# Optimization experiments

Hardware: AMD Instinct MI355X
Metric: run time of the kernel (lower is better)

Reference implementation:

```python
import jax, jax.numpy as jnp
import numpy as np

L, B, H, NI, V = 256, 32, 1024, 1024, 10000


def setup_inputs() -> dict:
    key = jax.random.key(0)
    ks = jax.random.split(key, 8)
    return {
        "input_ids": jax.random.randint(ks[0], (L, B), 0, V),
        "h0": jnp.zeros((B, H), jnp.float32),
        "c0": jnp.zeros((B, H), jnp.float32),
        "emb_w": jax.random.uniform(ks[1], (V, NI), jnp.float32, -0.1, 0.1),
        "w_ih": jax.random.normal(ks[2], (4 * H, NI), jnp.float32) * 0.02,
        "w_hh": jax.random.normal(ks[3], (4 * H, H), jnp.float32) * 0.02,
        "dec_w": jax.random.uniform(ks[4], (V, H), jnp.float32, -0.1, 0.1),
        "dec_b": jnp.zeros((V,), jnp.float32),
        "W": jax.random.normal(ks[5], (H, 1), jnp.float32) * 0.1,
        "U": jax.random.normal(ks[6], (H, 1), jnp.float32) * 0.1,
    }


def reference(input_ids, h0, c0, emb_w, w_ih, w_hh, dec_w, dec_b, W, U):
    seq_len, bsz = input_ids.shape
    nhid = h0.shape[1]
    emb = emb_w[input_ids]  # [L, B, NI]

    def lstm_cell(x, h, c):
        # torch LSTMCell (bias=False), gate order i, f, g, o
        gates = x @ w_ih.T + h @ w_hh.T  # [B, 4H]
        i, f, g, o = jnp.split(gates, 4, axis=-1)
        c_new = jax.nn.sigmoid(f) * c + jax.nn.sigmoid(i) * jnp.tanh(g)
        h_new = jax.nn.sigmoid(o) * jnp.tanh(c_new)
        return h_new, c_new

    time_idx = jnp.arange(seq_len)

    def step(carry, xs):
        h, c, hist = carry  # hist: [L, B, H] padded history of hiddens
        x, i = xs
        h, c = lstm_cell(x, h, c)
        hist = hist.at[i].set(h)
        # additive attention over all hiddens so far
        b = (hist.reshape(-1, nhid) @ U).reshape(seq_len, bsz)  # [L, B]
        a = (h @ W).reshape(1, bsz)  # [1, B]
        scores = jnp.tanh(a + b)
        scores = jnp.where((time_idx <= i)[:, None], scores, -jnp.inf)
        att = jax.nn.softmax(scores, axis=0)  # softmax over time
        ctx = jnp.sum(att[:, :, None] * hist, axis=0)  # [B, H]
        return (h, c, hist), ctx

    hist0 = jnp.zeros((seq_len, bsz, nhid), dtype=h0.dtype)
    (h, c, _), ctx = jax.lax.scan(step, (h0, c0, hist0), (emb, time_idx))
    # ctx: [L, B, H]
    logits = ctx @ dec_w.T + dec_b  # [L, B, V]
    out = jax.nn.log_softmax(logits, axis=-1)
    return out, (h, c)
```

## Files before the change

kernel.cpp:

```cpp
#include <hip/hip_runtime.h>
#include <math.h>

typedef unsigned short u16;
typedef unsigned u32;
typedef float f32x4 __attribute__((ext_vector_type(4)));
typedef float f32x2 __attribute__((ext_vector_type(2)));
typedef __bf16 bf16x8 __attribute__((ext_vector_type(8)));
typedef u16 u16x8 __attribute__((ext_vector_type(8)));
typedef u16 u16x4 __attribute__((ext_vector_type(4)));
typedef u32 u32x4 __attribute__((ext_vector_type(4)));

#define L_SEQ 256
#define BSZ 32
#define HID 1024
#define NIN 1024
#define VOC 10000
#define G4 4096
#define MROWS 8192
#define NB 64
#define DPB 16
#define SENT 0xFFFFFFFFu

__device__ __forceinline__ u16 f2bf(float f) {
    unsigned u = __float_as_uint(f);
    unsigned r = u + 0x7FFFu + ((u >> 16) & 1u);
    return (u16)(r >> 16);
}

__device__ __forceinline__ float fast_sigm(float x) {
    x = fminf(fmaxf(x, -15.f), 15.f);
    return __builtin_amdgcn_rcpf(1.f + __expf(-x));
}
__device__ __forceinline__ float fast_tanh(float x) {
    x = fminf(fmaxf(x, -15.f), 15.f);
    float t = __expf(2.f * x);
    return (t - 1.f) * __builtin_amdgcn_rcpf(t + 1.f);
}

__device__ __forceinline__ unsigned umax4(u16x8 v) {
    u32x4 c = __builtin_bit_cast(u32x4, v);
    unsigned a = c.x > c.y ? c.x : c.y;
    unsigned b = c.z > c.w ? c.z : c.w;
    return a > b ? a : b;
}

__global__ __launch_bounds__(256) void cvt_bf16_kernel(const float* __restrict__ in,
                                                       u16* __restrict__ out, int n4) {
    int idx = blockIdx.x * 256 + threadIdx.x;
    if (idx < n4) {
        f32x4 v = *(const f32x4*)(in + (size_t)idx * 4);
        u16x4 o = {f2bf(v.x), f2bf(v.y), f2bf(v.z), f2bf(v.w)};
        *(u16x4*)(out + (size_t)idx * 4) = o;
    }
}

__global__ __launch_bounds__(256) void gather_emb_kernel(const int* __restrict__ ids,
                                                         const float* __restrict__ emb_w,
                                                         u16* __restrict__ out) {
    int m = blockIdx.x;
    int id = ids[m];
    const float* src = emb_w + (size_t)id * NIN;
    u16* dst = out + (size_t)m * NIN;
    int t = threadIdx.x;
    f32x4 v = *(const f32x4*)(src + t * 4);
    u16x4 o = {f2bf(v.x), f2bf(v.y), f2bf(v.z), f2bf(v.w)};
    *(u16x4*)(dst + t * 4) = o;
}

__global__ __launch_bounds__(256) void gemm_bt_kernel(const u16* __restrict__ A,
                                                      const u16* __restrict__ B,
                                                      float* __restrict__ C,
                                                      const float* __restrict__ bias,
                                                      int M, int N, int K) {
    int m0 = blockIdx.x * 128;
    int n0 = blockIdx.y * 128;
    __shared__ alignas(16) u16 As[128][40];
    __shared__ alignas(16) u16 Bs[128][40];
    int t = threadIdx.x;
    int lane = t & 63, wave = t >> 6;
    int wr = wave >> 1, wc = wave & 1;
    int l15 = lane & 15, l4 = lane >> 4;

    f32x4 acc[4][4];
    f32x4 zv = {0.f, 0.f, 0.f, 0.f};
    for (int mi = 0; mi < 4; ++mi)
        for (int ni = 0; ni < 4; ++ni) acc[mi][ni] = zv;

    for (int k0 = 0; k0 < K; k0 += 32) {
        for (int s = 0; s < 2; ++s) {
            int task = t + s * 256;
            int row = task >> 2, kof = (task & 3) * 8;
            u16x8 av = *(const u16x8*)(A + (size_t)(m0 + row) * K + k0 + kof);
            *(u16x8*)(&As[row][kof]) = av;
            int brow = n0 + row;
            u16x8 bv = {0, 0, 0, 0, 0, 0, 0, 0};
            if (brow < N) bv = *(const u16x8*)(B + (size_t)brow * K + k0 + kof);
            *(u16x8*)(&Bs[row][kof]) = bv;
        }
        __syncthreads();
        bf16x8 af[4], bfr[4];
        for (int mi = 0; mi < 4; ++mi)
            af[mi] = __builtin_bit_cast(bf16x8, *(const u16x8*)(&As[wr * 64 + mi * 16 + l15][l4 * 8]));
        for (int ni = 0; ni < 4; ++ni)
            bfr[ni] = __builtin_bit_cast(bf16x8, *(const u16x8*)(&Bs[wc * 64 + ni * 16 + l15][l4 * 8]));
        for (int mi = 0; mi < 4; ++mi)
            for (int ni = 0; ni < 4; ++ni)
                acc[mi][ni] = __builtin_amdgcn_mfma_f32_16x16x32_bf16(af[mi], bfr[ni], acc[mi][ni], 0, 0, 0);
        __syncthreads();
    }

    for (int mi = 0; mi < 4; ++mi)
        for (int ni = 0; ni < 4; ++ni) {
            int col = n0 + wc * 64 + ni * 16 + l15;
            if (col < N) {
                float bb = bias ? bias[col] : 0.f;
                int rbase = m0 + wr * 64 + mi * 16 + l4 * 4;
                for (int r = 0; r < 4; ++r)
                    C[(size_t)(rbase + r) * N + col] = acc[mi][ni][r] + bb;
            }
        }
}


__global__ __launch_bounds__(256, 1) void lstm_seq_kernel(
    const float* __restrict__ c0, const u16* __restrict__ w_hh_bf,
    const float* __restrict__ gx, const float* __restrict__ Wv, const float* __restrict__ Uv,
    float* __restrict__ hist, u16* __restrict__ hb_hist, float* __restrict__ c_out,
    float* __restrict__ part_ab) {
    __shared__ alignas(16) u16 Bs[64][1024];
    __shared__ float gsm[4][32][16];
    __shared__ float c_sl[32][16];

    int blk = blockIdx.x;
    int d0 = blk * DPB;
    int t = threadIdx.x;
    int lane = t & 63, wave = t >> 6;
    int wm = wave & 1, wn = wave >> 1;
    int l15 = lane & 15, l4 = lane >> 4;

    for (int s = 0; s < 32; ++s) {
        int cid = t + s * 256;
        int c = cid >> 7;
        int ch = cid & 127;
        int g = c >> 4, dl = c & 15;
        u16x8 v = *(const u16x8*)(w_hh_bf + (size_t)(g * HID + d0 + dl) * HID + ch * 8);
        int chs = ch ^ (c & 7);
        *(u16x8*)(&Bs[c][chs * 8]) = v;
    }
    for (int s = t; s < 512; s += 256) {
        int b = s >> 4, dl = s & 15;
        c_sl[b][dl] = c0[b * HID + d0 + dl];
    }
    __syncthreads();

    int cA = wn * 32 + l15;
    int cB = cA + 16;
    int sw = cA & 7;
    int gA = cA >> 4, dA = cA & 15;
    int gB = cB >> 4, dB = cB & 15;

    int bb = t >> 3;
    int pr = t & 7;
    int dl0 = pr * 2;

    for (int i = 0; i < L_SEQ; ++i) {
        const u16* hb = hb_hist + (size_t)i * (BSZ * HID);
        const u16* aptr = hb + (size_t)(wm * 16 + l15) * HID + l4 * 8;

        float gxa[2][4];
#pragma unroll
        for (int r = 0; r < 4; ++r) {
            int m = wm * 16 + l4 * 4 + r;
            size_t rowb = (size_t)(i * BSZ + m) * G4;
            gxa[0][r] = gx[rowb + gA * HID + d0 + dA];
            gxa[1][r] = gx[rowb + gB * HID + d0 + dB];
        }

        u16x8 afr[32];
        unsigned needmask = 0xFFFFFFFFu;
        do {
#pragma unroll
            for (int kk = 0; kk < 32; ++kk)
                if (needmask & (1u << kk))
                    asm volatile("global_load_dwordx4 %0, %1, off offset:%c2 sc0 sc1"
                                 : "=v"(afr[kk])
                                 : "v"(aptr), "n"(kk * 64));
            asm volatile("s_waitcnt vmcnt(0)" ::: "memory");
            __builtin_amdgcn_sched_barrier(0);
            unsigned nm = 0;
#pragma unroll
            for (int kk = 0; kk < 32; ++kk)
                if (needmask & (1u << kk)) {
                    if (__ballot(umax4(afr[kk]) == SENT)) nm |= (1u << kk);
                }
            needmask = nm;
            if (needmask) __builtin_amdgcn_s_sleep(1);
        } while (needmask);
        __builtin_amdgcn_sched_barrier(0);

        f32x4 acc0 = {0.f, 0.f, 0.f, 0.f}, acc1 = {0.f, 0.f, 0.f, 0.f};
#pragma unroll
        for (int kk = 0; kk < 32; ++kk) {
            bf16x8 af = __builtin_bit_cast(bf16x8, afr[kk]);
            int ch = kk * 4 + l4;
            bf16x8 b0 = __builtin_bit_cast(bf16x8, *(const u16x8*)(&Bs[cA][(ch ^ sw) * 8]));
            bf16x8 b1 = __builtin_bit_cast(bf16x8, *(const u16x8*)(&Bs[cB][(ch ^ sw) * 8]));
            acc0 = __builtin_amdgcn_mfma_f32_16x16x32_bf16(af, b0, acc0, 0, 0, 0);
            acc1 = __builtin_amdgcn_mfma_f32_16x16x32_bf16(af, b1, acc1, 0, 0, 0);
        }

#pragma unroll
        for (int r = 0; r < 4; ++r) {
            int m = wm * 16 + l4 * 4 + r;
            gsm[gA][m][dA] = acc0[r] + gxa[0][r];
            gsm[gB][m][dB] = acc1[r] + gxa[1][r];
        }
        __syncthreads();

        u16* hb_next = hb_hist + (size_t)(i + 1) * (BSZ * HID);
        float hn01[2];
#pragma unroll
        for (int q = 0; q < 2; ++q) {
            int dl = dl0 + q;
            float ig = gsm[0][bb][dl], fg = gsm[1][bb][dl];
            float gg = gsm[2][bb][dl], og = gsm[3][bb][dl];
            float cn = fast_sigm(fg) * c_sl[bb][dl] + fast_sigm(ig) * fast_tanh(gg);
            float hn = fast_sigm(og) * fast_tanh(cn);
            c_sl[bb][dl] = cn;
            hn01[q] = hn;
        }
        unsigned pk = (unsigned)f2bf(hn01[0]) | ((unsigned)f2bf(hn01[1]) << 16);
        __hip_atomic_store((unsigned*)(hb_next + bb * HID + d0 + dl0), pk,
                           __ATOMIC_RELAXED, __HIP_MEMORY_SCOPE_AGENT);
        f32x2 hv = {hn01[0], hn01[1]};
        *(f32x2*)(hist + ((size_t)i * BSZ + bb) * HID + d0 + dl0) = hv;
        float pa = hn01[0] * Wv[d0 + dl0] + hn01[1] * Wv[d0 + dl0 + 1];
        float pb = hn01[0] * Uv[d0 + dl0] + hn01[1] * Uv[d0 + dl0 + 1];
        pa += __shfl_xor(pa, 1); pb += __shfl_xor(pb, 1);
        pa += __shfl_xor(pa, 2); pb += __shfl_xor(pb, 2);
        pa += __shfl_xor(pa, 4); pb += __shfl_xor(pb, 4);
        if (pr == 0) {
            f32x2 pv = {pa, pb};
            *(f32x2*)(part_ab + (((size_t)i * NB + blk) * BSZ + bb) * 2) = pv;
        }
    }

    for (int s = t; s < 512; s += 256) {
        int b2 = s >> 4, dl = s & 15;
        c_out[b2 * HID + d0 + dl] = c_sl[b2][dl];
    }
}

__global__ __launch_bounds__(256) void reduce_ab_kernel(const float* __restrict__ part_ab,
                                                        float* __restrict__ a_arr,
                                                        float* __restrict__ b_arr) {
    int i = blockIdx.x;
    int t = threadIdx.x;
    int b = t & 31, q = t >> 5;
    float sa = 0.f, sb = 0.f;
    for (int j = 0; j < 8; ++j) {
        int blk = q * 8 + j;
        f32x2 v = *(const f32x2*)(part_ab + (((size_t)i * NB + blk) * BSZ + b) * 2);
        sa += v.x;
        sb += v.y;
    }
    __shared__ float ra[8][32], rb[8][32];
    ra[q][b] = sa;
    rb[q][b] = sb;
    __syncthreads();
    if (q == 0) {
        for (int j = 1; j < 8; ++j) { sa += ra[j][b]; sb += rb[j][b]; }
        a_arr[i * BSZ + b] = sa;
        b_arr[i * BSZ + b] = sb;
    }
}

__global__ __launch_bounds__(256) void attn_kernel(const float* __restrict__ a_arr,
                                                   const float* __restrict__ b_arr,
                                                   const float* __restrict__ hist,
                                                   u16* __restrict__ ctx_bf) {
    int b = blockIdx.y;
    int i0 = blockIdx.x * 8;
    int t = threadIdx.x;
    __shared__ float att[8][256];
    __shared__ float red[256];

    float bt = b_arr[t * BSZ + b];
    for (int q = 0; q < 8; ++q) {
        int iq = i0 + q;
        att[q][t] = (t <= iq) ? tanhf(a_arr[iq * BSZ + b] + bt) : -INFINITY;
    }
    __syncthreads();
    for (int q = 0; q < 8; ++q) {
        int iq = i0 + q;
        red[t] = att[q][t];
        __syncthreads();
        for (int s = 128; s > 0; s >>= 1) {
            if (t < s) red[t] = fmaxf(red[t], red[t + s]);
            __syncthreads();
        }
        float m = red[0];
        __syncthreads();
        float e = (t <= iq) ? expf(att[q][t] - m) : 0.f;
        red[t] = e;
        __syncthreads();
        for (int s = 128; s > 0; s >>= 1) {
            if (t < s) red[t] += red[t + s];
            __syncthreads();
        }
        float sum = red[0];
        __syncthreads();
        att[q][t] = e / sum;
        __syncthreads();
    }

    int hc = t * 4;
    f32x4 accq[8];
    f32x4 zv = {0.f, 0.f, 0.f, 0.f};
    for (int q = 0; q < 8; ++q) accq[q] = zv;
    int imax = i0 + 7;
    for (int t2 = 0; t2 <= imax; ++t2) {
        f32x4 hv = *(const f32x4*)(hist + ((size_t)t2 * BSZ + b) * HID + hc);
        for (int q = 0; q < 8; ++q) accq[q] += hv * att[q][t2];
    }
    for (int q = 0; q < 8; ++q) {
        size_t row = (size_t)(i0 + q) * BSZ + b;
        u16x4 o = {f2bf(accq[q].x), f2bf(accq[q].y), f2bf(accq[q].z), f2bf(accq[q].w)};
        *(u16x4*)(ctx_bf + row * HID + hc) = o;
    }
}

__global__ __launch_bounds__(256) void logsoftmax_kernel(float* __restrict__ x, int V) {
    int row = blockIdx.x;
    float* p = x + (size_t)row * V;
    __shared__ float red[256];
    int t = threadIdx.x;
    float frag[40];
    float m = -INFINITY;
#pragma unroll
    for (int k = 0; k < 40; ++k) {
        int j = t + k * 256;
        if (j < VOC) {
            frag[k] = p[j];
            m = fmaxf(m, frag[k]);
        }
    }
    red[t] = m;
    __syncthreads();
    for (int s = 128; s > 0; s >>= 1) {
        if (t < s) red[t] = fmaxf(red[t], red[t + s]);
        __syncthreads();
    }
    m = red[0];
    __syncthreads();
    float sum = 0.f;
#pragma unroll
    for (int k = 0; k < 40; ++k) {
        int j = t + k * 256;
        if (j < VOC) sum += __expf(frag[k] - m);
    }
    red[t] = sum;
    __syncthreads();
    for (int s = 128; s > 0; s >>= 1) {
        if (t < s) red[t] += red[t + s];
        __syncthreads();
    }
    float lse = m + logf(red[0]);
#pragma unroll
    for (int k = 0; k < 40; ++k) {
        int j = t + k * 256;
        if (j < VOC) p[j] = frag[k] - lse;
    }
}

extern "C" void kernel_launch(void* const* d_in, const int* in_sizes, int n_in,
                              void* d_out, int out_size, void* d_ws, size_t ws_size,
                              hipStream_t stream) {
    const int* ids = (const int*)d_in[0];
    const float* h0 = (const float*)d_in[1];
    const float* c0 = (const float*)d_in[2];
    const float* emb_w = (const float*)d_in[3];
    const float* w_ih = (const float*)d_in[4];
    const float* w_hh = (const float*)d_in[5];
    const float* dec_w = (const float*)d_in[6];
    const float* dec_b = (const float*)d_in[7];
    const float* Wv = (const float*)d_in[8];
    const float* Uv = (const float*)d_in[9];

    char* p = (char*)d_ws;
    auto alloc = [&](size_t bytes) {
        void* r = (void*)p;
        p += (bytes + 255) & ~(size_t)255;
        return r;
    };
    u16* w_ih_bf = (u16*)alloc((size_t)G4 * NIN * 2);
    u16* w_hh_bf = (u16*)alloc((size_t)G4 * HID * 2);
    u16* dec_w_bf = (u16*)alloc((size_t)VOC * HID * 2);
    char* shared_region = (char*)alloc((size_t)(L_SEQ + 1) * BSZ * HID * 2);
    u16* A_emb = (u16*)shared_region;
    u16* hb_hist = (u16*)shared_region;
    u16* ctx_bf = (u16*)alloc((size_t)MROWS * HID * 2);
    float* hist = (float*)alloc((size_t)L_SEQ * BSZ * HID * 4);
    float* c_buf = (float*)alloc((size_t)BSZ * HID * 4);
    float* part_ab = (float*)alloc((size_t)L_SEQ * NB * BSZ * 2 * 4);
    float* a_arr = (float*)alloc((size_t)L_SEQ * BSZ * 4);
    float* b_arr = (float*)alloc((size_t)L_SEQ * BSZ * 4);

    float* out = (float*)d_out;
    float* gx = out;

    cvt_bf16_kernel<<<(G4 * NIN / 4 + 255) / 256, 256, 0, stream>>>(w_ih, w_ih_bf, G4 * NIN / 4);
    cvt_bf16_kernel<<<(G4 * HID / 4 + 255) / 256, 256, 0, stream>>>(w_hh, w_hh_bf, G4 * HID / 4);
    cvt_bf16_kernel<<<(VOC * HID / 4 + 255) / 256, 256, 0, stream>>>(dec_w, dec_w_bf, VOC * HID / 4);
    gather_emb_kernel<<<MROWS, 256, 0, stream>>>(ids, emb_w, A_emb);

    gemm_bt_kernel<<<dim3(MROWS / 128, G4 / 128), 256, 0, stream>>>(A_emb, w_ih_bf, gx, nullptr,
                                                                    MROWS, G4, NIN);
    hipMemsetAsync(hb_hist + (size_t)BSZ * HID, 0xFF, (size_t)L_SEQ * BSZ * HID * 2, stream);
    cvt_bf16_kernel<<<(BSZ * HID / 4 + 255) / 256, 256, 0, stream>>>(h0, hb_hist, BSZ * HID / 4);

    {
        const float* c0a = c0;
        const u16* whha = w_hh_bf;
        const float* gxa = gx;
        const float* Wa = Wv;
        const float* Ua = Uv;
        float* hista = hist;
        u16* hba = hb_hist;
        float* couta = c_buf;
        float* pab = part_ab;
        void* args[] = {&c0a, &whha, &gxa, &Wa, &Ua, &hista, &hba, &couta, &pab};
        hipLaunchCooperativeKernel((const void*)lstm_seq_kernel, dim3(NB), dim3(256), args, 0,
                                   stream);
    }
    reduce_ab_kernel<<<L_SEQ, 256, 0, stream>>>(part_ab, a_arr, b_arr);
    attn_kernel<<<dim3(L_SEQ / 8, BSZ), 256, 0, stream>>>(a_arr, b_arr, hist, ctx_bf);
    gemm_bt_kernel<<<dim3(MROWS / 128, (VOC + 127) / 128), 256, 0, stream>>>(ctx_bf, dec_w_bf, out,
                                                                             dec_b, MROWS, VOC, HID);
    logsoftmax_kernel<<<MROWS, 256, 0, stream>>>(out, VOC);
    hipMemcpyAsync(out + (size_t)MROWS * VOC, hist + (size_t)255 * BSZ * HID,
                   (size_t)BSZ * HID * 4, hipMemcpyDeviceToDevice, stream);
    hipMemcpyAsync(out + (size_t)MROWS * VOC + BSZ * HID, c_buf,
                   (size_t)BSZ * HID * 4, hipMemcpyDeviceToDevice, stream);
}
```

Before: 2.642 ms.

## Transpose input-gate GEMM output per block and read bf16 hidden history in attention

The input projection GEMM now writes its result in a blocked layout keyed by (d-block, step, gate, d, batch), so each lane in the sequential LSTM kernel loads four gate inputs with one vector load instead of scattered strided loads. The fp32 hidden-history buffer is dropped. The attention kernel reads the bf16 history already produced for the recurrence, and final h and c are written straight into the output tail, which removes two memcpys and a large fp32 store each step. Using bf16 hidden states in the context sum lowers accuracy slightly.

```diff
diff --git a/kernel.cpp b/kernel.cpp
--- a/kernel.cpp
+++ b/kernel.cpp
@@ -26,6 +26,7 @@
     unsigned r = u + 0x7FFFu + ((u >> 16) & 1u);
     return (u16)(r >> 16);
 }
+#define BF2F(x) __builtin_bit_cast(float, (u32)((u16)(x)) << 16)
 
 __device__ __forceinline__ float fast_sigm(float x) {
     x = fminf(fmaxf(x, -15.f), 15.f);
@@ -36,7 +37,6 @@
     float t = __expf(2.f * x);
     return (t - 1.f) * __builtin_amdgcn_rcpf(t + 1.f);
 }
-
 __device__ __forceinline__ unsigned umax4(u16x8 v) {
     u32x4 c = __builtin_bit_cast(u32x4, v);
     unsigned a = c.x > c.y ? c.x : c.y;
@@ -65,6 +65,53 @@
     f32x4 v = *(const f32x4*)(src + t * 4);
     u16x4 o = {f2bf(v.x), f2bf(v.y), f2bf(v.z), f2bf(v.w)};
     *(u16x4*)(dst + t * 4) = o;
+}
+
+__global__ __launch_bounds__(256) void gemm_gxT_kernel(const u16* __restrict__ A,
+                                                       const u16* __restrict__ B,
+                                                       float* __restrict__ gxT) {
+    int m0 = blockIdx.x * 128;
+    int n0 = blockIdx.y * 128;
+    __shared__ alignas(16) u16 As[128][40];
+    __shared__ alignas(16) u16 Bs[128][40];
+    int t = threadIdx.x;
+    int lane = t & 63, wave = t >> 6;
+    int wr = wave >> 1, wc = wave & 1;
+    int l15 = lane & 15, l4 = lane >> 4;
+
+    f32x4 acc[4][4];
+    f32x4 zv = {0.f, 0.f, 0.f, 0.f};
+    for (int mi = 0; mi < 4; ++mi)
+        for (int ni = 0; ni < 4; ++ni) acc[mi][ni] = zv;
+
+    for (int k0 = 0; k0 < NIN; k0 += 32) {
+        for (int s = 0; s < 2; ++s) {
+            int task = t + s * 256;
+            int row = task >> 2, kof = (task & 3) * 8;
+            *(u16x8*)(&As[row][kof]) = *(const u16x8*)(A + (size_t)(m0 + row) * NIN + k0 + kof);
+            *(u16x8*)(&Bs[row][kof]) = *(const u16x8*)(B + (size_t)(n0 + row) * NIN + k0 + kof);
+        }
+        __syncthreads();
+        bf16x8 af[4], bfr[4];
+        for (int mi = 0; mi < 4; ++mi)
+            af[mi] = __builtin_bit_cast(bf16x8, *(const u16x8*)(&As[wr * 64 + mi * 16 + l15][l4 * 8]));
+        for (int ni = 0; ni < 4; ++ni)
+            bfr[ni] = __builtin_bit_cast(bf16x8, *(const u16x8*)(&Bs[wc * 64 + ni * 16 + l15][l4 * 8]));
+        for (int mi = 0; mi < 4; ++mi)
+            for (int ni = 0; ni < 4; ++ni)
+                acc[mi][ni] = __builtin_amdgcn_mfma_f32_16x16x32_bf16(af[mi], bfr[ni], acc[mi][ni], 0, 0, 0);
+        __syncthreads();
+    }
+    for (int mi = 0; mi < 4; ++mi)
+        for (int ni = 0; ni < 4; ++ni) {
+            int n = n0 + wc * 64 + ni * 16 + l15;
+            int g = n >> 10, dd = n & 1023;
+            int dblk = dd >> 4, dl = dd & 15;
+            int mbase = m0 + wr * 64 + mi * 16 + l4 * 4;
+            int i = mbase >> 5, bb = mbase & 31;
+            size_t idx = ((((size_t)dblk * L_SEQ + i) * 4 + g) * 16 + dl) * 32 + bb;
+            *(f32x4*)(&gxT[idx]) = acc[mi][ni];
+        }
 }
 
 __global__ __launch_bounds__(256) void gemm_bt_kernel(const u16* __restrict__ A,
@@ -121,12 +168,10 @@
         }
 }
 
-
 __global__ __launch_bounds__(256, 1) void lstm_seq_kernel(
     const float* __restrict__ c0, const u16* __restrict__ w_hh_bf,
-    const float* __restrict__ gx, const float* __restrict__ Wv, const float* __restrict__ Uv,
-    float* __restrict__ hist, u16* __restrict__ hb_hist, float* __restrict__ c_out,
-    float* __restrict__ part_ab) {
+    const float* __restrict__ gxT, const float* __restrict__ Wv, const float* __restrict__ Uv,
+    u16* __restrict__ hb_hist, float* __restrict__ out_tail, float* __restrict__ part_ab) {
     __shared__ alignas(16) u16 Bs[64][1024];
     __shared__ float gsm[4][32][16];
     __shared__ float c_sl[32][16];
@@ -163,18 +208,14 @@
     int pr = t & 7;
     int dl0 = pr * 2;
 
+    const float* gxTb = gxT + (size_t)blk * ((size_t)L_SEQ * 2048) + wm * 16 + l4 * 4;
+
     for (int i = 0; i < L_SEQ; ++i) {
         const u16* hb = hb_hist + (size_t)i * (BSZ * HID);
         const u16* aptr = hb + (size_t)(wm * 16 + l15) * HID + l4 * 8;
 
-        float gxa[2][4];
-#pragma unroll
-        for (int r = 0; r < 4; ++r) {
-            int m = wm * 16 + l4 * 4 + r;
-            size_t rowb = (size_t)(i * BSZ + m) * G4;
-            gxa[0][r] = gx[rowb + gA * HID + d0 + dA];
-            gxa[1][r] = gx[rowb + gB * HID + d0 + dB];
-        }
+        f32x4 gxa0 = *(const f32x4*)(gxTb + (size_t)i * 2048 + gA * 512 + dA * 32);
+        f32x4 gxa1 = *(const f32x4*)(gxTb + (size_t)i * 2048 + gB * 512 + dB * 32);
 
         u16x8 afr[32];
         unsigned needmask = 0xFFFFFFFFu;
@@ -212,8 +253,8 @@
 #pragma unroll
         for (int r = 0; r < 4; ++r) {
             int m = wm * 16 + l4 * 4 + r;
-            gsm[gA][m][dA] = acc0[r] + gxa[0][r];
-            gsm[gB][m][dB] = acc1[r] + gxa[1][r];
+            gsm[gA][m][dA] = acc0[r] + gxa0[r];
+            gsm[gB][m][dB] = acc1[r] + gxa1[r];
         }
         __syncthreads();
 
@@ -232,8 +273,10 @@
         unsigned pk = (unsigned)f2bf(hn01[0]) | ((unsigned)f2bf(hn01[1]) << 16);
         __hip_atomic_store((unsigned*)(hb_next + bb * HID + d0 + dl0), pk,
                            __ATOMIC_RELAXED, __HIP_MEMORY_SCOPE_AGENT);
-        f32x2 hv = {hn01[0], hn01[1]};
-        *(f32x2*)(hist + ((size_t)i * BSZ + bb) * HID + d0 + dl0) = hv;
+        if (i == L_SEQ - 1) {
+            f32x2 hv = {hn01[0], hn01[1]};
+            *(f32x2*)(out_tail + (size_t)bb * HID + d0 + dl0) = hv;
+        }
         float pa = hn01[0] * Wv[d0 + dl0] + hn01[1] * Wv[d0 + dl0 + 1];
         float pb = hn01[0] * Uv[d0 + dl0] + hn01[1] * Uv[d0 + dl0 + 1];
         pa += __shfl_xor(pa, 1); pb += __shfl_xor(pb, 1);
@@ -247,7 +290,7 @@
 
     for (int s = t; s < 512; s += 256) {
         int b2 = s >> 4, dl = s & 15;
-        c_out[b2 * HID + d0 + dl] = c_sl[b2][dl];
+        out_tail[(size_t)BSZ * HID + b2 * HID + d0 + dl] = c_sl[b2][dl];
     }
 }
 
@@ -277,7 +320,7 @@
 
 __global__ __launch_bounds__(256) void attn_kernel(const float* __restrict__ a_arr,
                                                    const float* __restrict__ b_arr,
-                                                   const float* __restrict__ hist,
+                                                   const u16* __restrict__ hb_hist,
                                                    u16* __restrict__ ctx_bf) {
     int b = blockIdx.y;
     int i0 = blockIdx.x * 8;
@@ -320,7 +363,8 @@
     for (int q = 0; q < 8; ++q) accq[q] = zv;
     int imax = i0 + 7;
     for (int t2 = 0; t2 <= imax; ++t2) {
-        f32x4 hv = *(const f32x4*)(hist + ((size_t)t2 * BSZ + b) * HID + hc);
+        u16x4 hq = *(const u16x4*)(hb_hist + (size_t)(t2 + 1) * (BSZ * HID) + (size_t)b * HID + hc);
+        f32x4 hv = {BF2F(hq.x), BF2F(hq.y), BF2F(hq.z), BF2F(hq.w)};
         for (int q = 0; q < 8; ++q) accq[q] += hv * att[q][t2];
     }
     for (int q = 0; q < 8; ++q) {
@@ -396,50 +440,43 @@
     u16* w_ih_bf = (u16*)alloc((size_t)G4 * NIN * 2);
     u16* w_hh_bf = (u16*)alloc((size_t)G4 * HID * 2);
     u16* dec_w_bf = (u16*)alloc((size_t)VOC * HID * 2);
-    char* shared_region = (char*)alloc((size_t)(L_SEQ + 1) * BSZ * HID * 2);
-    u16* A_emb = (u16*)shared_region;
-    u16* hb_hist = (u16*)shared_region;
+    char* hbreg = (char*)alloc((size_t)(L_SEQ + 1) * BSZ * HID * 2);
     u16* ctx_bf = (u16*)alloc((size_t)MROWS * HID * 2);
-    float* hist = (float*)alloc((size_t)L_SEQ * BSZ * HID * 4);
-    float* c_buf = (float*)alloc((size_t)BSZ * HID * 4);
     float* part_ab = (float*)alloc((size_t)L_SEQ * NB * BSZ * 2 * 4);
     float* a_arr = (float*)alloc((size_t)L_SEQ * BSZ * 4);
     float* b_arr = (float*)alloc((size_t)L_SEQ * BSZ * 4);
 
+    u16* A_emb = (u16*)hbreg;
+    u16* hb_hist = (u16*)hbreg;
     float* out = (float*)d_out;
-    float* gx = out;
-
-    cvt_bf16_kernel<<<(G4 * NIN / 4 + 255) / 256, 256, 0, stream>>>(w_ih, w_ih_bf, G4 * NIN / 4);
-    cvt_bf16_kernel<<<(G4 * HID / 4 + 255) / 256, 256, 0, stream>>>(w_hh, w_hh_bf, G4 * HID / 4);
+    float* gxT = out;
+    float* out_tail = out + (size_t)MROWS * VOC;
+
+    cvt_bf16_kernel<<<G4 * NIN / 1024, 256, 0, stream>>>(w_ih, w_ih_bf, G4 * NIN / 4);
+    cvt_bf16_kernel<<<G4 * HID / 1024, 256, 0, stream>>>(w_hh, w_hh_bf, G4 * HID / 4);
     cvt_bf16_kernel<<<(VOC * HID / 4 + 255) / 256, 256, 0, stream>>>(dec_w, dec_w_bf, VOC * HID / 4);
     gather_emb_kernel<<<MROWS, 256, 0, stream>>>(ids, emb_w, A_emb);
-
-    gemm_bt_kernel<<<dim3(MROWS / 128, G4 / 128), 256, 0, stream>>>(A_emb, w_ih_bf, gx, nullptr,
-                                                                    MROWS, G4, NIN);
+    gemm_gxT_kernel<<<dim3(MROWS / 128, G4 / 128), 256, 0, stream>>>(A_emb, w_ih_bf, gxT);
+
     hipMemsetAsync(hb_hist + (size_t)BSZ * HID, 0xFF, (size_t)L_SEQ * BSZ * HID * 2, stream);
-    cvt_bf16_kernel<<<(BSZ * HID / 4 + 255) / 256, 256, 0, stream>>>(h0, hb_hist, BSZ * HID / 4);
+    cvt_bf16_kernel<<<BSZ * HID / 1024, 256, 0, stream>>>(h0, hb_hist, BSZ * HID / 4);
 
     {
         const float* c0a = c0;
         const u16* whha = w_hh_bf;
-        const float* gxa = gx;
+        const float* gxa = gxT;
         const float* Wa = Wv;
         const float* Ua = Uv;
-        float* hista = hist;
         u16* hba = hb_hist;
-        float* couta = c_buf;
+        float* tail = out_tail;
         float* pab = part_ab;
-        void* args[] = {&c0a, &whha, &gxa, &Wa, &Ua, &hista, &hba, &couta, &pab};
+        void* args[] = {&c0a, &whha, &gxa, &Wa, &Ua, &hba, &tail, &pab};
         hipLaunchCooperativeKernel((const void*)lstm_seq_kernel, dim3(NB), dim3(256), args, 0,
                                    stream);
     }
     reduce_ab_kernel<<<L_SEQ, 256, 0, stream>>>(part_ab, a_arr, b_arr);
-    attn_kernel<<<dim3(L_SEQ / 8, BSZ), 256, 0, stream>>>(a_arr, b_arr, hist, ctx_bf);
+    attn_kernel<<<dim3(L_SEQ / 8, BSZ), 256, 0, stream>>>(a_arr, b_arr, hb_hist, ctx_bf);
     gemm_bt_kernel<<<dim3(MROWS / 128, (VOC + 127) / 128), 256, 0, stream>>>(ctx_bf, dec_w_bf, out,
                                                                              dec_b, MROWS, VOC, HID);
     logsoftmax_kernel<<<MROWS, 256, 0, stream>>>(out, VOC);
-    hipMemcpyAsync(out + (size_t)MROWS * VOC, hist + (size_t)255 * BSZ * HID,
-                   (size_t)BSZ * HID * 4, hipMemcpyDeviceToDevice, stream);
-    hipMemcpyAsync(out + (size_t)MROWS * VOC + BSZ * HID, c_buf,
-                   (size_t)BSZ * HID * 4, hipMemcpyDeviceToDevice, stream);
-}
+}
```

New measurement: 2.587 ms. -2.1%, faster.
